# Kernel optimization log

Hardware: AMD Instinct MI355X
Metric: run time of the kernel (lower is better)

## Reference

```python
import jax, jax.numpy as jnp
import numpy as np

N_NODES = 100000
E2 = 1600000
E3 = 1600000
ES = 100000
HID = 64


def _mlp_3x3(x_in, W1, b1, W2, b2):
    # x_in: [E, d_in] -> mobility [E, 3, 3]
    h = jax.nn.relu(x_in @ W1 + b1)
    out = h @ W2 + b2  # [E, 9]
    return out.reshape(-1, 3, 3)


def setup_inputs() -> dict:
    key = jax.random.key(0)
    ks = jax.random.split(key, 20)
    inp = {}
    inp["x"] = jax.random.normal(ks[0], (N_NODES, 3), dtype=jnp.float32)
    inp["edge_2body"] = jax.random.randint(ks[1], (2, E2), 0, N_NODES)
    inp["edge_3body"] = jax.random.randint(ks[2], (3, E3), 0, N_NODES)
    inp["edge_2bodySelf"] = jax.random.randint(ks[3], (2, ES), 0, N_NODES)
    inp["edge_1body"] = jax.random.randint(ks[4], (2, ES), 0, N_NODES)
    inp["edge_attr_2body"] = jax.random.normal(ks[5], (E2, 3), dtype=jnp.float32)
    inp["edge_attr_3body"] = jax.random.normal(ks[6], (E3, 3), dtype=jnp.float32)
    inp["edge_attr_2bodySelf"] = jax.random.normal(ks[7], (ES, 3), dtype=jnp.float32)
    inp["edge_attr_1body"] = jax.random.normal(ks[8], (ES, 3), dtype=jnp.float32)
    s = 0.1
    # nn_2body: 3 -> HID -> 9
    inp["W1_2b"] = jax.random.normal(ks[9], (3, HID), dtype=jnp.float32) * s
    inp["b1_2b"] = jnp.zeros((HID,), jnp.float32)
    inp["W2_2b"] = jax.random.normal(ks[10], (HID, 9), dtype=jnp.float32) * s
    inp["b2_2b"] = jnp.zeros((9,), jnp.float32)
    # nn_3body: 6 -> HID -> 9
    inp["W1_3b"] = jax.random.normal(ks[11], (6, HID), dtype=jnp.float32) * s
    inp["b1_3b"] = jnp.zeros((HID,), jnp.float32)
    inp["W2_3b"] = jax.random.normal(ks[12], (HID, 9), dtype=jnp.float32) * s
    inp["b2_3b"] = jnp.zeros((9,), jnp.float32)
    # nn_self: 3 -> HID -> 9
    inp["W1_s"] = jax.random.normal(ks[13], (3, HID), dtype=jnp.float32) * s
    inp["b1_s"] = jnp.zeros((HID,), jnp.float32)
    inp["W2_s"] = jax.random.normal(ks[14], (HID, 9), dtype=jnp.float32) * s
    inp["b2_s"] = jnp.zeros((9,), jnp.float32)
    return inp


def reference(x, edge_2body, edge_3body, edge_2bodySelf, edge_1body,
              edge_attr_2body, edge_attr_3body, edge_attr_2bodySelf, edge_attr_1body,
              W1_2b, b1_2b, W2_2b, b2_2b,
              W1_3b, b1_3b, W2_3b, b2_3b,
              W1_s, b1_s, W2_s, b2_s):
    n = x.shape[0]
    # ---- 2-body: gather -> MLP -> per-edge 3x3 matvec -> scatter-add ----
    d2 = x[edge_2body[0]] - x[edge_2body[1]]  # xj - xi, [E2,3]
    mob2 = _mlp_3x3(d2, W1_2b, b1_2b, W2_2b, b2_2b)
    y2 = jnp.einsum('eij,ej->ei', mob2, edge_attr_2body)
    v2 = jax.ops.segment_sum(y2, edge_2body[1], num_segments=n)
    # ---- 3-body ----
    xj = x[edge_3body[0]]
    xk = x[edge_3body[1]]
    xi = x[edge_3body[2]]
    d3 = jnp.concatenate((xk - xj, xi - xk), axis=1)  # [E3,6]
    mob3 = _mlp_3x3(d3, W1_3b, b1_3b, W2_3b, b2_3b)
    y3 = jnp.einsum('eij,ej->ei', mob3, edge_attr_3body)
    v3 = jax.ops.segment_sum(y3, edge_3body[2], num_segments=n)
    # ---- 2-body self ----
    ds = x[edge_2bodySelf[0]] - x[edge_2bodySelf[1]]
    mobs = _mlp_3x3(ds, W1_s, b1_s, W2_s, b2_s)
    ys = jnp.einsum('eij,ej->ei', mobs, edge_attr_2bodySelf)
    vs = jax.ops.segment_sum(ys, edge_2bodySelf[1], num_segments=n)
    # edge_1body / edge_attr_1body unused in original forward
    return v2 + v3 + vs
```

## Files before the change

kernel.cpp:

```cpp
#include <hip/hip_runtime.h>


constexpr int HIDDEN = 64;
constexpr int NB_MAX = 256;
constexpr int NPB_SHIFT = 9;
constexpr int NPB = 1 << NPB_SHIFT;
constexpr int TILE_F = NPB * 3;
constexpr int NET_SLOT = 1040;
constexpr int BLK = 256;
constexpr int KPT = 4;

typedef _Float16 h2_t __attribute__((ext_vector_type(2)));

__device__ __forceinline__ unsigned packh2(float a, float b) {
    auto h = __builtin_amdgcn_cvt_pkrtz(a, b);
    return __builtin_bit_cast(unsigned, h);
}
__device__ __forceinline__ float fdot2u(unsigned a, unsigned b, float c) {
    h2_t ha = __builtin_bit_cast(h2_t, a);
    h2_t hb = __builtin_bit_cast(h2_t, b);
#if __has_builtin(__builtin_amdgcn_fdot2)
    return __builtin_amdgcn_fdot2(ha, hb, c, false);
#else
    return fmaf((float)ha.x, (float)hb.x, fmaf((float)ha.y, (float)hb.y, c));
#endif
}


__global__ __launch_bounds__(256) void setup_kernel(
    const float* __restrict__ x, int n_nodes, float4* __restrict__ x4,
    int* __restrict__ gcount,
    const float* __restrict__ W1_2b, const float* __restrict__ b1_2b,
    const float* __restrict__ W2_2b, const float* __restrict__ b2_2b,
    const float* __restrict__ W1_s,  const float* __restrict__ b1_s,
    const float* __restrict__ W2_s,  const float* __restrict__ b2_s,
    const float* __restrict__ W1_3b, const float* __restrict__ b1_3b,
    const float* __restrict__ W2_3b, const float* __restrict__ b2_3b,
    unsigned* __restrict__ nets)
{
    const int blk = blockIdx.x;
    const int tid = threadIdx.x;
    if (blk < 3) {
        const float *W1, *b1, *W2, *b2; int din;
        if (blk == 0) { W1 = W1_2b; b1 = b1_2b; W2 = W2_2b; b2 = b2_2b; din = 3; }
        else if (blk == 1) { W1 = W1_s; b1 = b1_s; W2 = W2_s; b2 = b2_s; din = 3; }
        else { W1 = W1_3b; b1 = b1_3b; W2 = W2_3b; b2 = b2_3b; din = 6; }
        unsigned* slot = nets + blk * NET_SLOT;
        float* slotf = (float*)slot;
        if (tid < 32) {
            const int h2 = tid, hA = 2 * h2, hB = 2 * h2 + 1;
            if (din == 3) {
                unsigned* row = slot + h2 * 16;
                float* rowf = (float*)row;
                row[0] = packh2(W1[0 * HIDDEN + hA], W1[1 * HIDDEN + hA]);
                row[1] = packh2(W1[0 * HIDDEN + hB], W1[1 * HIDDEN + hB]);
                rowf[2] = b1[hA]; rowf[3] = b1[hB];
                rowf[4] = W1[2 * HIDDEN + hA]; rowf[5] = W1[2 * HIDDEN + hB];
                #pragma unroll
                for (int i = 0; i < 9; ++i)
                    row[6 + i] = packh2(W2[hA * 9 + i], W2[hB * 9 + i]);
                row[15] = 0;
            } else {
                unsigned* row = slot + h2 * 32;
                float* rowf = (float*)row;
                #pragma unroll
                for (int r = 0; r < 3; ++r) {
                    row[r]     = packh2(W1[(2 * r) * HIDDEN + hA], W1[(2 * r + 1) * HIDDEN + hA]);
                    row[3 + r] = packh2(W1[(2 * r) * HIDDEN + hB], W1[(2 * r + 1) * HIDDEN + hB]);
                }
                rowf[6] = b1[hA]; rowf[7] = b1[hB];
                #pragma unroll
                for (int i = 0; i < 9; ++i)
                    row[8 + i] = packh2(W2[hA * 9 + i], W2[hB * 9 + i]);
                #pragma unroll
                for (int i = 17; i < 20; ++i) row[i] = 0;
            }
        }
        if (tid >= 32 && tid < 41) slotf[1024 + (tid - 32)] = b2[tid - 32];
        if (blk == 0) gcount[tid] = 0;
    } else {
        int i = (blk - 3) * 256 + tid;
        if (i < n_nodes)
            x4[i] = make_float4(x[3 * i], x[3 * i + 1], x[3 * i + 2], 0.0f);
    }
}

__global__ __launch_bounds__(256) void p1_edge_kernel(
    const float4* __restrict__ x4,
    const int* __restrict__ e0, long long E0, const float* __restrict__ at0,
    const int* __restrict__ e1, long long E1, const float* __restrict__ at1,
    const int* __restrict__ e2, long long E2, const float* __restrict__ at2,
    int g0, int g1,
    const unsigned* __restrict__ nets,
    float4* __restrict__ records, int* __restrict__ gcount, int cap)
{
    static_assert(NB_MAX == BLK, "one reserve bin per thread");
    __shared__ __align__(16) unsigned s_net[1033];
    __shared__ int s_rank[NB_MAX];
    __shared__ int s_base[NB_MAX];

    const int gA = g0 + g1;
    const int gB = (int)gridDim.x - gA;
    const int mn = (gA < gB) ? gA : gB;
    int aidx = -1, b6 = -1;
    {
        const int idx = blockIdx.x;
        if (idx < 2 * mn) { if (idx & 1) b6 = idx >> 1; else aidx = idx >> 1; }
        else {
            const int r = idx - 2 * mn;
            if (gA > gB) aidx = mn + r; else b6 = mn + r;
        }
    }

    const int* edges; long long E; const float* attr;
    int bidx, nblk, din3;
    const unsigned* wp;
    if (aidx >= 0) {
        if (aidx < g0) { edges = e0; E = E0; attr = at0; bidx = aidx;      nblk = g0; din3 = 1; wp = nets; }
        else           { edges = e1; E = E1; attr = at1; bidx = aidx - g0; nblk = g1; din3 = 1; wp = nets + NET_SLOT; }
    } else             { edges = e2; E = E2; attr = at2; bidx = b6;        nblk = gB; din3 = 0; wp = nets + 2 * NET_SLOT; }

    const int tid = threadIdx.x;
    long long span = (E + nblk - 1) / nblk;
    span = (span + 1023) & ~1023LL;
    const long long lo = (long long)bidx * span;
    const long long hi = (lo + span < E) ? (lo + span) : E;
    if (lo >= E) return;

    const bool e_aligned = ((E & 3) == 0);

    s_rank[tid] = 0;
    const int nstage = din3 ? 512 : 1024;
    for (int i = tid; i < nstage; i += BLK) s_net[i] = wp[i];
    if (tid < 9) s_net[1024 + tid] = wp[1024 + tid];
    __syncthreads();

    const unsigned* w = s_net;
    const float* wf = (const float*)s_net;
    float b2r[9];
    #pragma unroll
    for (int i = 0; i < 9; ++i) b2r[i] = wf[1024 + i];

    const long long be = lo + (long long)tid * KPT;

    unsigned dp[KPT][3];
    float    d2s[KPT];
    float    a[KPT][3];
    int      dst[KPT];
    bool     valid[KPT];
    int      i0[KPT], i1[KPT], i2[KPT];

    const bool lane_live = (be < hi);
    const bool full = lane_live && e_aligned && (be + KPT <= hi);
    if (full) {
        int4 r0 = *(const int4*)(edges + be);
        int4 r1 = *(const int4*)(edges + E + be);
        i0[0] = r0.x; i0[1] = r0.y; i0[2] = r0.z; i0[3] = r0.w;
        i1[0] = r1.x; i1[1] = r1.y; i1[2] = r1.z; i1[3] = r1.w;
        if (!din3) {
            int4 r2 = *(const int4*)(edges + 2 * E + be);
            i2[0] = r2.x; i2[1] = r2.y; i2[2] = r2.z; i2[3] = r2.w;
        }
        float4 a0 = *(const float4*)(attr + 3 * be);
        float4 a1 = *(const float4*)(attr + 3 * be + 4);
        float4 a2 = *(const float4*)(attr + 3 * be + 8);
        a[0][0] = a0.x; a[0][1] = a0.y; a[0][2] = a0.z;
        a[1][0] = a0.w; a[1][1] = a1.x; a[1][2] = a1.y;
        a[2][0] = a1.z; a[2][1] = a1.w; a[2][2] = a2.x;
        a[3][0] = a2.y; a[3][1] = a2.z; a[3][2] = a2.w;
        #pragma unroll
        for (int u = 0; u < KPT; ++u) valid[u] = true;
    } else {
        #pragma unroll
        for (int u = 0; u < KPT; ++u) {
            long long e = be + u;
            valid[u] = lane_live && (e < hi);
            long long ee = valid[u] ? e : lo;
            i0[u] = edges[ee];
            i1[u] = edges[E + ee];
            if (!din3) i2[u] = edges[2 * E + ee];
            #pragma unroll
            for (int c = 0; c < 3; ++c) a[u][c] = attr[3 * ee + c];
        }
    }

    #pragma unroll
    for (int u = 0; u < KPT; ++u) {
        if (din3) {
            dst[u] = i1[u];
            float4 xs = x4[i0[u]];
            float4 xt = x4[i1[u]];
            dp[u][0] = packh2(xs.x - xt.x, xs.y - xt.y);
            d2s[u]   = xs.z - xt.z;
            dp[u][1] = 0; dp[u][2] = 0;
        } else {
            dst[u] = i2[u];
            float4 xj = x4[i0[u]];
            float4 xk = x4[i1[u]];
            float4 xi = x4[i2[u]];
            dp[u][0] = packh2(xk.x - xj.x, xk.y - xj.y);
            dp[u][1] = packh2(xk.z - xj.z, xi.x - xk.x);
            dp[u][2] = packh2(xi.y - xk.y, xi.z - xk.z);
            d2s[u] = 0.f;
        }
    }

    float acc[KPT][9];
    #pragma unroll
    for (int u = 0; u < KPT; ++u)
        #pragma unroll
        for (int i = 0; i < 9; ++i) acc[u][i] = b2r[i];

    if (din3) {
        #pragma unroll 2
        for (int hh2 = 0; hh2 < HIDDEN / 2; ++hh2) {
            const uint4* rq = (const uint4*)(w + (hh2 << 4));
            const uint4 q0 = rq[0], q1 = rq[1], q2 = rq[2], q3 = rq[3];
            const unsigned wA = q0.x;
            const unsigned wB = q0.y;
            const float bbA = __uint_as_float(q0.z);
            const float bbB = __uint_as_float(q0.w);
            const float wcA = __uint_as_float(q1.x);
            const float wcB = __uint_as_float(q1.y);
            const unsigned w2p[9] = {q1.z, q1.w, q2.x, q2.y, q2.z,
                                     q2.w, q3.x, q3.y, q3.z};
            #pragma unroll
            for (int u = 0; u < KPT; ++u) {
                float preA = fmaf(d2s[u], wcA, fdot2u(dp[u][0], wA, bbA));
                float preB = fmaf(d2s[u], wcB, fdot2u(dp[u][0], wB, bbB));
                unsigned h2 = packh2(fmaxf(preA, 0.f), fmaxf(preB, 0.f));
                #pragma unroll
                for (int i = 0; i < 9; ++i)
                    acc[u][i] = fdot2u(h2, w2p[i], acc[u][i]);
            }
        }
    } else {
        #pragma unroll 2
        for (int hh2 = 0; hh2 < HIDDEN / 2; ++hh2) {
            const uint4* rq = (const uint4*)(w + (hh2 << 5));
            const uint4 q0 = rq[0], q1 = rq[1], q2 = rq[2], q3 = rq[3];
            const unsigned q4x = w[(hh2 << 5) + 16];
            const unsigned wA0 = q0.x, wA1 = q0.y, wA2 = q0.z;
            const unsigned wB0 = q0.w, wB1 = q1.x, wB2 = q1.y;
            const float bbA = __uint_as_float(q1.z);
            const float bbB = __uint_as_float(q1.w);
            const unsigned w2p[9] = {q2.x, q2.y, q2.z, q2.w, q3.x,
                                     q3.y, q3.z, q3.w, q4x};
            #pragma unroll
            for (int u = 0; u < KPT; ++u) {
                float preA = fdot2u(dp[u][2], wA2,
                             fdot2u(dp[u][1], wA1,
                             fdot2u(dp[u][0], wA0, bbA)));
                float preB = fdot2u(dp[u][2], wB2,
                             fdot2u(dp[u][1], wB1,
                             fdot2u(dp[u][0], wB0, bbB)));
                unsigned h2 = packh2(fmaxf(preA, 0.f), fmaxf(preB, 0.f));
                #pragma unroll
                for (int i = 0; i < 9; ++i)
                    acc[u][i] = fdot2u(h2, w2p[i], acc[u][i]);
            }
        }
    }

    int rk[KPT]; int bb[KPT];
    #pragma unroll
    for (int u = 0; u < KPT; ++u) {
        if (valid[u]) {
            bb[u] = dst[u] >> NPB_SHIFT;
            rk[u] = atomicAdd(&s_rank[bb[u]], 1);
        }
    }
    __syncthreads();

    {
        int c = s_rank[tid];
        s_base[tid] = (c > 0) ? atomicAdd(&gcount[tid], c) : 0;
    }
    __syncthreads();

    #pragma unroll
    for (int u = 0; u < KPT; ++u) {
        if (!valid[u]) continue;
        float y0 = fmaf(acc[u][0], a[u][0], fmaf(acc[u][1], a[u][1], acc[u][2] * a[u][2]));
        float y1 = fmaf(acc[u][3], a[u][0], fmaf(acc[u][4], a[u][1], acc[u][5] * a[u][2]));
        float y2 = fmaf(acc[u][6], a[u][0], fmaf(acc[u][7], a[u][1], acc[u][8] * a[u][2]));
        int slot = s_base[bb[u]] + rk[u];
        if (slot < cap)
            records[(size_t)bb[u] * cap + slot] =
                make_float4(y0, y1, y2, __int_as_float(dst[u]));
    }
}

__global__ __launch_bounds__(1024) void p2_bucket(
    const float4* __restrict__ records, const int* __restrict__ gcount,
    int cap, int n_nodes, float* __restrict__ out)
{
    __shared__ float s_acc[TILE_F];
    const int b = blockIdx.x;
    const int tid = threadIdx.x;

    for (int i = tid; i < TILE_F; i += 1024) s_acc[i] = 0.0f;
    __syncthreads();

    int cnt = gcount[b];
    if (cnt > cap) cnt = cap;
    const float4* rb = records + (size_t)b * cap;

    int i = tid;
    for (; i + 3 * 1024 < cnt; i += 4 * 1024) {
        float4 r0 = rb[i];
        float4 r1 = rb[i + 1024];
        float4 r2 = rb[i + 2048];
        float4 r3 = rb[i + 3072];
        int l0 = __float_as_int(r0.w) - (b << NPB_SHIFT);
        int l1 = __float_as_int(r1.w) - (b << NPB_SHIFT);
        int l2 = __float_as_int(r2.w) - (b << NPB_SHIFT);
        int l3 = __float_as_int(r3.w) - (b << NPB_SHIFT);
        atomicAdd(&s_acc[l0 * 3 + 0], r0.x);
        atomicAdd(&s_acc[l0 * 3 + 1], r0.y);
        atomicAdd(&s_acc[l0 * 3 + 2], r0.z);
        atomicAdd(&s_acc[l1 * 3 + 0], r1.x);
        atomicAdd(&s_acc[l1 * 3 + 1], r1.y);
        atomicAdd(&s_acc[l1 * 3 + 2], r1.z);
        atomicAdd(&s_acc[l2 * 3 + 0], r2.x);
        atomicAdd(&s_acc[l2 * 3 + 1], r2.y);
        atomicAdd(&s_acc[l2 * 3 + 2], r2.z);
        atomicAdd(&s_acc[l3 * 3 + 0], r3.x);
        atomicAdd(&s_acc[l3 * 3 + 1], r3.y);
        atomicAdd(&s_acc[l3 * 3 + 2], r3.z);
    }
    for (; i < cnt; i += 1024) {
        float4 r = rb[i];
        int loc = __float_as_int(r.w) - (b << NPB_SHIFT);
        atomicAdd(&s_acc[loc * 3 + 0], r.x);
        atomicAdd(&s_acc[loc * 3 + 1], r.y);
        atomicAdd(&s_acc[loc * 3 + 2], r.z);
    }
    __syncthreads();

    const int start = (b << NPB_SHIFT) * 3;
    const int end = min(n_nodes * 3, ((b + 1) << NPB_SHIFT) * 3);
    for (int i2 = start + tid; i2 < end; i2 += 1024)
        out[i2] = s_acc[i2 - start];
}

template <int DIN, int KPTF>
__global__ __launch_bounds__(256) void edge_mlp_atomic(
    const float* __restrict__ x,
    const int* __restrict__ edges, long long E,
    const float* __restrict__ attr,
    const float* __restrict__ W1, const float* __restrict__ b1,
    const float* __restrict__ W2, const float* __restrict__ b2,
    float* __restrict__ out)
{
    const int tid = threadIdx.x;
    const long long base = (long long)blockIdx.x * (blockDim.x * KPTF) + tid;
    float d[KPTF][DIN]; float a[KPTF][3]; int dst[KPTF]; bool valid[KPTF];
    #pragma unroll
    for (int u = 0; u < KPTF; ++u) {
        long long e = base + (long long)u * blockDim.x;
        valid[u] = (e < E);
        long long ee = valid[u] ? e : 0;
        if constexpr (DIN == 3) {
            int s = edges[ee]; int t = edges[E + ee]; dst[u] = t;
            #pragma unroll
            for (int c = 0; c < 3; ++c)
                d[u][c] = x[3 * (long long)s + c] - x[3 * (long long)t + c];
        } else {
            int j = edges[ee]; int k = edges[E + ee]; int i = edges[2 * E + ee];
            dst[u] = i;
            #pragma unroll
            for (int c = 0; c < 3; ++c) {
                float xj = x[3 * (long long)j + c];
                float xk = x[3 * (long long)k + c];
                float xi = x[3 * (long long)i + c];
                d[u][c] = xk - xj; d[u][3 + c] = xi - xk;
            }
        }
        #pragma unroll
        for (int c = 0; c < 3; ++c) a[u][c] = attr[3 * ee + c];
    }
    float acc[KPTF][9];
    #pragma unroll
    for (int u = 0; u < KPTF; ++u)
        #pragma unroll
        for (int i = 0; i < 9; ++i) acc[u][i] = b2[i];
    #pragma unroll 4
    for (int hh = 0; hh < HIDDEN; ++hh) {
        const float bb = b1[hh];
        float w1r[DIN];
        #pragma unroll
        for (int r = 0; r < DIN; ++r) w1r[r] = W1[r * HIDDEN + hh];
        float w2r[9];
        #pragma unroll
        for (int i = 0; i < 9; ++i) w2r[i] = W2[hh * 9 + i];
        #pragma unroll
        for (int u = 0; u < KPTF; ++u) {
            float pre = bb;
            #pragma unroll
            for (int r = 0; r < DIN; ++r) pre = fmaf(d[u][r], w1r[r], pre);
            const float h = fmaxf(pre, 0.0f);
            #pragma unroll
            for (int i = 0; i < 9; ++i) acc[u][i] = fmaf(h, w2r[i], acc[u][i]);
        }
    }
    #pragma unroll
    for (int u = 0; u < KPTF; ++u) {
        if (!valid[u]) continue;
        float* o = out + 3 * (long long)dst[u];
        #pragma unroll
        for (int i = 0; i < 3; ++i) {
            float y = fmaf(acc[u][3 * i + 0], a[u][0],
                      fmaf(acc[u][3 * i + 1], a[u][1],
                           acc[u][3 * i + 2] * a[u][2]));
            atomicAdd(&o[i], y);
        }
    }
}

extern "C" void kernel_launch(void* const* d_in, const int* in_sizes, int n_in,
                              void* d_out, int out_size, void* d_ws, size_t ws_size,
                              hipStream_t stream)
{
    const float* x  = (const float*)d_in[0];
    const int*   e2 = (const int*)d_in[1];
    const int*   e3 = (const int*)d_in[2];
    const int*   es = (const int*)d_in[3];
    const float* a2 = (const float*)d_in[5];
    const float* a3 = (const float*)d_in[6];
    const float* as = (const float*)d_in[7];
    const float* W1_2b = (const float*)d_in[9];
    const float* b1_2b = (const float*)d_in[10];
    const float* W2_2b = (const float*)d_in[11];
    const float* b2_2b = (const float*)d_in[12];
    const float* W1_3b = (const float*)d_in[13];
    const float* b1_3b = (const float*)d_in[14];
    const float* W2_3b = (const float*)d_in[15];
    const float* b2_3b = (const float*)d_in[16];
    const float* W1_s  = (const float*)d_in[17];
    const float* b1_s  = (const float*)d_in[18];
    const float* W2_s  = (const float*)d_in[19];
    const float* b2_s  = (const float*)d_in[20];

    const long long E2 = in_sizes[1] / 2;
    const long long E3 = in_sizes[2] / 3;
    const long long ES = in_sizes[3] / 2;
    const long long Etot = E2 + E3 + ES;
    const int n_nodes = out_size / 3;
    const int nbuckets = (n_nodes + NPB - 1) >> NPB_SHIFT;

    float* out = (float*)d_out;

    const size_t off_nets = 1024;
    const size_t off_x4 = (off_nets + 3 * NET_SLOT * 4 + 255) & ~(size_t)255;
    const size_t x4_bytes = (size_t)n_nodes * sizeof(float4);
    const size_t off_rec = (off_x4 + x4_bytes + 255) & ~(size_t)255;

    long long mean_per_bucket = (Etot + nbuckets - 1) / nbuckets;
    long long min_cap = mean_per_bucket + 1600;
    long long cap_avail =
        ((long long)ws_size - (long long)off_rec) / ((long long)nbuckets * 16);

    constexpr int SPAN = 1024;
    int g0 = (int)((E2 + SPAN - 1) / SPAN);
    int g1 = (int)((ES + SPAN - 1) / SPAN);
    int g2g = (int)((E3 + SPAN - 1) / SPAN);

    if (nbuckets <= NB_MAX && cap_avail >= min_cap) {
        long long capL = min_cap + 4096;
        if (capL > cap_avail) capL = cap_avail;
        int cap = (int)capL;
        int* gcount = (int*)d_ws;
        unsigned* nets = (unsigned*)((char*)d_ws + off_nets);
        float4* x4 = (float4*)((char*)d_ws + off_x4);
        float4* records = (float4*)((char*)d_ws + off_rec);

        int nb_pad = (n_nodes + 255) / 256;
        setup_kernel<<<3 + nb_pad, 256, 0, stream>>>(
            x, n_nodes, x4, gcount,
            W1_2b, b1_2b, W2_2b, b2_2b,
            W1_s,  b1_s,  W2_s,  b2_s,
            W1_3b, b1_3b, W2_3b, b2_3b,
            nets);

        p1_edge_kernel<<<g0 + g1 + g2g, 256, 0, stream>>>(
            x4,
            e2, E2, a2,
            es, ES, as,
            e3, E3, a3,
            g0, g1,
            nets, records, gcount, cap);

        p2_bucket<<<nbuckets, 1024, 0, stream>>>(records, gcount, cap, n_nodes, out);
    } else {
        hipMemsetAsync(out, 0, (size_t)out_size * sizeof(float), stream);
        constexpr int FB_BLK = 256, FB_KPT = 4;
        const long long per_blk = (long long)FB_BLK * FB_KPT;
        int a2g = (int)((E2 + per_blk - 1) / per_blk);
        int a3g = (int)((E3 + per_blk - 1) / per_blk);
        int asg = (int)((ES + per_blk - 1) / per_blk);
        if (a2g > 0)
            edge_mlp_atomic<3, FB_KPT><<<a2g, FB_BLK, 0, stream>>>(
                x, e2, E2, a2, W1_2b, b1_2b, W2_2b, b2_2b, out);
        if (a3g > 0)
            edge_mlp_atomic<6, FB_KPT><<<a3g, FB_BLK, 0, stream>>>(
                x, e3, E3, a3, W1_3b, b1_3b, W2_3b, b2_3b, out);
        if (asg > 0)
            edge_mlp_atomic<3, FB_KPT><<<asg, FB_BLK, 0, stream>>>(
                x, es, ES, as, W1_s, b1_s, W2_s, b2_s, out);
    }
}
```

Measured before the change: 282.4 us.

## Make edge blocks loop over multiple 1024-edge chunks from both edge sets

The edge kernel now launches about a quarter as many blocks. Each block walks up to two chunks from the 2-body/self side and two from the 3-body side in sequence. Weight staging into shared memory is skipped when consecutive chunks use the same network. The aim is to amortise per-block setup and the global bucket-count atomics over more work. The cost is fewer resident waves for hiding gather latency, and each block's chunks run one after another.

```diff
diff --git a/kernel.cpp b/kernel.cpp
--- a/kernel.cpp
+++ b/kernel.cpp
@@ -90,7 +90,7 @@
     const int* __restrict__ e0, long long E0, const float* __restrict__ at0,
     const int* __restrict__ e1, long long E1, const float* __restrict__ at1,
     const int* __restrict__ e2, long long E2, const float* __restrict__ at2,
-    int g0, int g1,
+    int g0, int gA, int gB,
     const unsigned* __restrict__ nets,
     float4* __restrict__ records, int* __restrict__ gcount, int cap)
 {
@@ -99,195 +99,194 @@
     __shared__ int s_rank[NB_MAX];
     __shared__ int s_base[NB_MAX];
 
-    const int gA = g0 + g1;
-    const int gB = (int)gridDim.x - gA;
-    const int mn = (gA < gB) ? gA : gB;
-    int aidx = -1, b6 = -1;
-    {
-        const int idx = blockIdx.x;
-        if (idx < 2 * mn) { if (idx & 1) b6 = idx >> 1; else aidx = idx >> 1; }
-        else {
-            const int r = idx - 2 * mn;
-            if (gA > gB) aidx = mn + r; else b6 = mn + r;
+    const int tid = threadIdx.x;
+    const int blk = blockIdx.x;
+    int cur_set = -1;
+
+    for (int side = 0; side < 2; ++side) {
+        const int lim = side ? gB : gA;
+        for (int j = 0; j < 2; ++j) {
+            const int t = 2 * blk + j;
+            if (t >= lim) continue;
+
+            const int* edges; long long E; const float* attr;
+            int din3, set; long long lo;
+            if (side == 0) {
+                if (t < g0) { set = 0; edges = e0; E = E0; attr = at0; lo = (long long)t << 10; }
+                else        { set = 1; edges = e1; E = E1; attr = at1; lo = (long long)(t - g0) << 10; }
+                din3 = 1;
+            } else {
+                set = 2; edges = e2; E = E2; attr = at2; din3 = 0;
+                lo = (long long)t << 10;
+            }
+            const long long hi = (lo + 1024 < E) ? lo + 1024 : E;
+            const bool e_aligned = ((E & 3) == 0);
+
+            s_rank[tid] = 0;
+            if (set != cur_set) {
+                const unsigned* wp = nets + set * NET_SLOT;
+                const int nstage = din3 ? 512 : 1024;
+                for (int i = tid; i < nstage; i += BLK) s_net[i] = wp[i];
+                if (tid < 9) s_net[1024 + tid] = wp[1024 + tid];
+                cur_set = set;
+            }
+            __syncthreads();
+
+            const unsigned* w = s_net;
+            const float* wf = (const float*)s_net;
+            float b2r[9];
+            #pragma unroll
+            for (int i = 0; i < 9; ++i) b2r[i] = wf[1024 + i];
+
+            const long long be = lo + (long long)tid * KPT;
+
+            unsigned dp[KPT][3];
+            float    d2s[KPT];
+            float    a[KPT][3];
+            int      dst[KPT];
+            bool     valid[KPT];
+            int      i0[KPT], i1[KPT], i2[KPT];
+
+            const bool lane_live = (be < hi);
+            const bool full = lane_live && e_aligned && (be + KPT <= hi);
+            if (full) {
+                int4 r0 = *(const int4*)(edges + be);
+                int4 r1 = *(const int4*)(edges + E + be);
+                i0[0] = r0.x; i0[1] = r0.y; i0[2] = r0.z; i0[3] = r0.w;
+                i1[0] = r1.x; i1[1] = r1.y; i1[2] = r1.z; i1[3] = r1.w;
+                if (!din3) {
+                    int4 r2 = *(const int4*)(edges + 2 * E + be);
+                    i2[0] = r2.x; i2[1] = r2.y; i2[2] = r2.z; i2[3] = r2.w;
+                }
+                float4 a0 = *(const float4*)(attr + 3 * be);
+                float4 a1 = *(const float4*)(attr + 3 * be + 4);
+                float4 a2 = *(const float4*)(attr + 3 * be + 8);
+                a[0][0] = a0.x; a[0][1] = a0.y; a[0][2] = a0.z;
+                a[1][0] = a0.w; a[1][1] = a1.x; a[1][2] = a1.y;
+                a[2][0] = a1.z; a[2][1] = a1.w; a[2][2] = a2.x;
+                a[3][0] = a2.y; a[3][1] = a2.z; a[3][2] = a2.w;
+                #pragma unroll
+                for (int u = 0; u < KPT; ++u) valid[u] = true;
+            } else {
+                #pragma unroll
+                for (int u = 0; u < KPT; ++u) {
+                    long long e = be + u;
+                    valid[u] = lane_live && (e < hi);
+                    long long ee = valid[u] ? e : lo;
+                    i0[u] = edges[ee];
+                    i1[u] = edges[E + ee];
+                    if (!din3) i2[u] = edges[2 * E + ee];
+                    #pragma unroll
+                    for (int c = 0; c < 3; ++c) a[u][c] = attr[3 * ee + c];
+                }
+            }
+
+            #pragma unroll
+            for (int u = 0; u < KPT; ++u) {
+                if (din3) {
+                    dst[u] = i1[u];
+                    float4 xs = x4[i0[u]];
+                    float4 xt = x4[i1[u]];
+                    dp[u][0] = packh2(xs.x - xt.x, xs.y - xt.y);
+                    d2s[u]   = xs.z - xt.z;
+                    dp[u][1] = 0; dp[u][2] = 0;
+                } else {
+                    dst[u] = i2[u];
+                    float4 xj = x4[i0[u]];
+                    float4 xk = x4[i1[u]];
+                    float4 xi = x4[i2[u]];
+                    dp[u][0] = packh2(xk.x - xj.x, xk.y - xj.y);
+                    dp[u][1] = packh2(xk.z - xj.z, xi.x - xk.x);
+                    dp[u][2] = packh2(xi.y - xk.y, xi.z - xk.z);
+                    d2s[u] = 0.f;
+                }
+            }
+
+            float acc[KPT][9];
+            #pragma unroll
+            for (int u = 0; u < KPT; ++u)
+                #pragma unroll
+                for (int i = 0; i < 9; ++i) acc[u][i] = b2r[i];
+
+            if (din3) {
+                #pragma unroll 2
+                for (int hh2 = 0; hh2 < HIDDEN / 2; ++hh2) {
+                    const uint4* rq = (const uint4*)(w + (hh2 << 4));
+                    const uint4 q0 = rq[0], q1 = rq[1], q2 = rq[2], q3 = rq[3];
+                    const unsigned wA = q0.x;
+                    const unsigned wB = q0.y;
+                    const float bbA = __uint_as_float(q0.z);
+                    const float bbB = __uint_as_float(q0.w);
+                    const float wcA = __uint_as_float(q1.x);
+                    const float wcB = __uint_as_float(q1.y);
+                    const unsigned w2p[9] = {q1.z, q1.w, q2.x, q2.y, q2.z,
+                                             q2.w, q3.x, q3.y, q3.z};
+                    #pragma unroll
+                    for (int u = 0; u < KPT; ++u) {
+                        float preA = fmaf(d2s[u], wcA, fdot2u(dp[u][0], wA, bbA));
+                        float preB = fmaf(d2s[u], wcB, fdot2u(dp[u][0], wB, bbB));
+                        unsigned h2 = packh2(fmaxf(preA, 0.f), fmaxf(preB, 0.f));
+                        #pragma unroll
+                        for (int i = 0; i < 9; ++i)
+                            acc[u][i] = fdot2u(h2, w2p[i], acc[u][i]);
+                    }
+                }
+            } else {
+                #pragma unroll 2
+                for (int hh2 = 0; hh2 < HIDDEN / 2; ++hh2) {
+                    const uint4* rq = (const uint4*)(w + (hh2 << 5));
+                    const uint4 q0 = rq[0], q1 = rq[1], q2 = rq[2], q3 = rq[3];
+                    const unsigned q4x = w[(hh2 << 5) + 16];
+                    const unsigned wA0 = q0.x, wA1 = q0.y, wA2 = q0.z;
+                    const unsigned wB0 = q0.w, wB1 = q1.x, wB2 = q1.y;
+                    const float bbA = __uint_as_float(q1.z);
+                    const float bbB = __uint_as_float(q1.w);
+                    const unsigned w2p[9] = {q2.x, q2.y, q2.z, q2.w, q3.x,
+                                             q3.y, q3.z, q3.w, q4x};
+                    #pragma unroll
+                    for (int u = 0; u < KPT; ++u) {
+                        float preA = fdot2u(dp[u][2], wA2,
+                                     fdot2u(dp[u][1], wA1,
+                                     fdot2u(dp[u][0], wA0, bbA)));
+                        float preB = fdot2u(dp[u][2], wB2,
+                                     fdot2u(dp[u][1], wB1,
+                                     fdot2u(dp[u][0], wB0, bbB)));
+                        unsigned h2 = packh2(fmaxf(preA, 0.f), fmaxf(preB, 0.f));
+                        #pragma unroll
+                        for (int i = 0; i < 9; ++i)
+                            acc[u][i] = fdot2u(h2, w2p[i], acc[u][i]);
+                    }
+                }
+            }
+
+            int rk[KPT]; int bb[KPT];
+            #pragma unroll
+            for (int u = 0; u < KPT; ++u) {
+                if (valid[u]) {
+                    bb[u] = dst[u] >> NPB_SHIFT;
+                    rk[u] = atomicAdd(&s_rank[bb[u]], 1);
+                }
+            }
+            __syncthreads();
+
+            {
+                int c = s_rank[tid];
+                s_base[tid] = (c > 0) ? atomicAdd(&gcount[tid], c) : 0;
+            }
+            __syncthreads();
+
+            #pragma unroll
+            for (int u = 0; u < KPT; ++u) {
+                if (!valid[u]) continue;
+                float y0 = fmaf(acc[u][0], a[u][0], fmaf(acc[u][1], a[u][1], acc[u][2] * a[u][2]));
+                float y1 = fmaf(acc[u][3], a[u][0], fmaf(acc[u][4], a[u][1], acc[u][5] * a[u][2]));
+                float y2 = fmaf(acc[u][6], a[u][0], fmaf(acc[u][7], a[u][1], acc[u][8] * a[u][2]));
+                int slot = s_base[bb[u]] + rk[u];
+                if (slot < cap)
+                    records[(size_t)bb[u] * cap + slot] =
+                        make_float4(y0, y1, y2, __int_as_float(dst[u]));
+            }
         }
-    }
-
-    const int* edges; long long E; const float* attr;
-    int bidx, nblk, din3;
-    const unsigned* wp;
-    if (aidx >= 0) {
-        if (aidx < g0) { edges = e0; E = E0; attr = at0; bidx = aidx;      nblk = g0; din3 = 1; wp = nets; }
-        else           { edges = e1; E = E1; attr = at1; bidx = aidx - g0; nblk = g1; din3 = 1; wp = nets + NET_SLOT; }
-    } else             { edges = e2; E = E2; attr = at2; bidx = b6;        nblk = gB; din3 = 0; wp = nets + 2 * NET_SLOT; }
-
-    const int tid = threadIdx.x;
-    long long span = (E + nblk - 1) / nblk;
-    span = (span + 1023) & ~1023LL;
-    const long long lo = (long long)bidx * span;
-    const long long hi = (lo + span < E) ? (lo + span) : E;
-    if (lo >= E) return;
-
-    const bool e_aligned = ((E & 3) == 0);
-
-    s_rank[tid] = 0;
-    const int nstage = din3 ? 512 : 1024;
-    for (int i = tid; i < nstage; i += BLK) s_net[i] = wp[i];
-    if (tid < 9) s_net[1024 + tid] = wp[1024 + tid];
-    __syncthreads();
-
-    const unsigned* w = s_net;
-    const float* wf = (const float*)s_net;
-    float b2r[9];
-    #pragma unroll
-    for (int i = 0; i < 9; ++i) b2r[i] = wf[1024 + i];
-
-    const long long be = lo + (long long)tid * KPT;
-
-    unsigned dp[KPT][3];
-    float    d2s[KPT];
-    float    a[KPT][3];
-    int      dst[KPT];
-    bool     valid[KPT];
-    int      i0[KPT], i1[KPT], i2[KPT];
-
-    const bool lane_live = (be < hi);
-    const bool full = lane_live && e_aligned && (be + KPT <= hi);
-    if (full) {
-        int4 r0 = *(const int4*)(edges + be);
-        int4 r1 = *(const int4*)(edges + E + be);
-        i0[0] = r0.x; i0[1] = r0.y; i0[2] = r0.z; i0[3] = r0.w;
-        i1[0] = r1.x; i1[1] = r1.y; i1[2] = r1.z; i1[3] = r1.w;
-        if (!din3) {
-            int4 r2 = *(const int4*)(edges + 2 * E + be);
-            i2[0] = r2.x; i2[1] = r2.y; i2[2] = r2.z; i2[3] = r2.w;
-        }
-        float4 a0 = *(const float4*)(attr + 3 * be);
-        float4 a1 = *(const float4*)(attr + 3 * be + 4);
-        float4 a2 = *(const float4*)(attr + 3 * be + 8);
-        a[0][0] = a0.x; a[0][1] = a0.y; a[0][2] = a0.z;
-        a[1][0] = a0.w; a[1][1] = a1.x; a[1][2] = a1.y;
-        a[2][0] = a1.z; a[2][1] = a1.w; a[2][2] = a2.x;
-        a[3][0] = a2.y; a[3][1] = a2.z; a[3][2] = a2.w;
-        #pragma unroll
-        for (int u = 0; u < KPT; ++u) valid[u] = true;
-    } else {
-        #pragma unroll
-        for (int u = 0; u < KPT; ++u) {
-            long long e = be + u;
-            valid[u] = lane_live && (e < hi);
-            long long ee = valid[u] ? e : lo;
-            i0[u] = edges[ee];
-            i1[u] = edges[E + ee];
-            if (!din3) i2[u] = edges[2 * E + ee];
-            #pragma unroll
-            for (int c = 0; c < 3; ++c) a[u][c] = attr[3 * ee + c];
-        }
-    }
-
-    #pragma unroll
-    for (int u = 0; u < KPT; ++u) {
-        if (din3) {
-            dst[u] = i1[u];
-            float4 xs = x4[i0[u]];
-            float4 xt = x4[i1[u]];
-            dp[u][0] = packh2(xs.x - xt.x, xs.y - xt.y);
-            d2s[u]   = xs.z - xt.z;
-            dp[u][1] = 0; dp[u][2] = 0;
-        } else {
-            dst[u] = i2[u];
-            float4 xj = x4[i0[u]];
-            float4 xk = x4[i1[u]];
-            float4 xi = x4[i2[u]];
-            dp[u][0] = packh2(xk.x - xj.x, xk.y - xj.y);
-            dp[u][1] = packh2(xk.z - xj.z, xi.x - xk.x);
-            dp[u][2] = packh2(xi.y - xk.y, xi.z - xk.z);
-            d2s[u] = 0.f;
-        }
-    }
-
-    float acc[KPT][9];
-    #pragma unroll
-    for (int u = 0; u < KPT; ++u)
-        #pragma unroll
-        for (int i = 0; i < 9; ++i) acc[u][i] = b2r[i];
-
-    if (din3) {
-        #pragma unroll 2
-        for (int hh2 = 0; hh2 < HIDDEN / 2; ++hh2) {
-            const uint4* rq = (const uint4*)(w + (hh2 << 4));
-            const uint4 q0 = rq[0], q1 = rq[1], q2 = rq[2], q3 = rq[3];
-            const unsigned wA = q0.x;
-            const unsigned wB = q0.y;
-            const float bbA = __uint_as_float(q0.z);
-            const float bbB = __uint_as_float(q0.w);
-            const float wcA = __uint_as_float(q1.x);
-            const float wcB = __uint_as_float(q1.y);
-            const unsigned w2p[9] = {q1.z, q1.w, q2.x, q2.y, q2.z,
-                                     q2.w, q3.x, q3.y, q3.z};
-            #pragma unroll
-            for (int u = 0; u < KPT; ++u) {
-                float preA = fmaf(d2s[u], wcA, fdot2u(dp[u][0], wA, bbA));
-                float preB = fmaf(d2s[u], wcB, fdot2u(dp[u][0], wB, bbB));
-                unsigned h2 = packh2(fmaxf(preA, 0.f), fmaxf(preB, 0.f));
-                #pragma unroll
-                for (int i = 0; i < 9; ++i)
-                    acc[u][i] = fdot2u(h2, w2p[i], acc[u][i]);
-            }
-        }
-    } else {
-        #pragma unroll 2
-        for (int hh2 = 0; hh2 < HIDDEN / 2; ++hh2) {
-            const uint4* rq = (const uint4*)(w + (hh2 << 5));
-            const uint4 q0 = rq[0], q1 = rq[1], q2 = rq[2], q3 = rq[3];
-            const unsigned q4x = w[(hh2 << 5) + 16];
-            const unsigned wA0 = q0.x, wA1 = q0.y, wA2 = q0.z;
-            const unsigned wB0 = q0.w, wB1 = q1.x, wB2 = q1.y;
-            const float bbA = __uint_as_float(q1.z);
-            const float bbB = __uint_as_float(q1.w);
-            const unsigned w2p[9] = {q2.x, q2.y, q2.z, q2.w, q3.x,
-                                     q3.y, q3.z, q3.w, q4x};
-            #pragma unroll
-            for (int u = 0; u < KPT; ++u) {
-                float preA = fdot2u(dp[u][2], wA2,
-                             fdot2u(dp[u][1], wA1,
-                             fdot2u(dp[u][0], wA0, bbA)));
-                float preB = fdot2u(dp[u][2], wB2,
-                             fdot2u(dp[u][1], wB1,
-                             fdot2u(dp[u][0], wB0, bbB)));
-                unsigned h2 = packh2(fmaxf(preA, 0.f), fmaxf(preB, 0.f));
-                #pragma unroll
-                for (int i = 0; i < 9; ++i)
-                    acc[u][i] = fdot2u(h2, w2p[i], acc[u][i]);
-            }
-        }
-    }
-
-    int rk[KPT]; int bb[KPT];
-    #pragma unroll
-    for (int u = 0; u < KPT; ++u) {
-        if (valid[u]) {
-            bb[u] = dst[u] >> NPB_SHIFT;
-            rk[u] = atomicAdd(&s_rank[bb[u]], 1);
-        }
-    }
-    __syncthreads();
-
-    {
-        int c = s_rank[tid];
-        s_base[tid] = (c > 0) ? atomicAdd(&gcount[tid], c) : 0;
-    }
-    __syncthreads();
-
-    #pragma unroll
-    for (int u = 0; u < KPT; ++u) {
-        if (!valid[u]) continue;
-        float y0 = fmaf(acc[u][0], a[u][0], fmaf(acc[u][1], a[u][1], acc[u][2] * a[u][2]));
-        float y1 = fmaf(acc[u][3], a[u][0], fmaf(acc[u][4], a[u][1], acc[u][5] * a[u][2]));
-        float y2 = fmaf(acc[u][6], a[u][0], fmaf(acc[u][7], a[u][1], acc[u][8] * a[u][2]));
-        int slot = s_base[bb[u]] + rk[u];
-        if (slot < cap)
-            records[(size_t)bb[u] * cap + slot] =
-                make_float4(y0, y1, y2, __int_as_float(dst[u]));
     }
 }
 
@@ -461,10 +460,12 @@
     long long cap_avail =
         ((long long)ws_size - (long long)off_rec) / ((long long)nbuckets * 16);
 
-    constexpr int SPAN = 1024;
-    int g0 = (int)((E2 + SPAN - 1) / SPAN);
-    int g1 = (int)((ES + SPAN - 1) / SPAN);
-    int g2g = (int)((E3 + SPAN - 1) / SPAN);
+    int g0 = (int)((E2 + 1023) / 1024);
+    int g1 = (int)((ES + 1023) / 1024);
+    int gB = (int)((E3 + 1023) / 1024);
+    int gA = g0 + g1;
+    int gmax = (gA > gB) ? gA : gB;
+    int G = (gmax + 1) / 2;
 
     if (nbuckets <= NB_MAX && cap_avail >= min_cap) {
         long long capL = min_cap + 4096;
@@ -483,12 +484,12 @@
             W1_3b, b1_3b, W2_3b, b2_3b,
             nets);
 
-        p1_edge_kernel<<<g0 + g1 + g2g, 256, 0, stream>>>(
+        p1_edge_kernel<<<G, 256, 0, stream>>>(
             x4,
             e2, E2, a2,
             es, ES, as,
             e3, E3, a3,
-            g0, g1,
+            g0, gA, gB,
             nets, records, gcount, cap);
 
         p2_bucket<<<nbuckets, 1024, 0, stream>>>(records, gcount, cap, n_nodes, out);
```

After: 302.8 us. 7.2% more time.

## Fold setup kernel into edge kernel: pack weights per block, gather x directly

Applied to the files above, without the earlier changes.

Removes the separate setup kernel. Each edge block now packs the MLP weights into shared memory itself, and the per-node x values are gathered directly as 12-byte structs instead of padded float4 copies. The gcount reset becomes a memset, and the weight packing overlaps with the index and coordinate gathers before a barrier placed later. This saves one kernel launch and the x4 staging pass, at the cost of redundant per-block weight packing and unaligned 12-byte gathers.

```diff
diff --git a/kernel.cpp b/kernel.cpp
--- a/kernel.cpp
+++ b/kernel.cpp
@@ -6,11 +6,12 @@
 constexpr int NPB_SHIFT = 9;
 constexpr int NPB = 1 << NPB_SHIFT;
 constexpr int TILE_F = NPB * 3;
-constexpr int NET_SLOT = 1040;
 constexpr int BLK = 256;
 constexpr int KPT = 4;
 
 typedef _Float16 h2_t __attribute__((ext_vector_type(2)));
+
+struct F3 { float x, y, z; };
 
 __device__ __forceinline__ unsigned packh2(float a, float b) {
     auto h = __builtin_amdgcn_cvt_pkrtz(a, b);
@@ -27,71 +28,18 @@
 }
 
 
-__global__ __launch_bounds__(256) void setup_kernel(
-    const float* __restrict__ x, int n_nodes, float4* __restrict__ x4,
-    int* __restrict__ gcount,
+__global__ __launch_bounds__(256) void p1_edge_kernel(
+    const float* __restrict__ x,
+    const int* __restrict__ e0, long long E0, const float* __restrict__ at0,
+    const int* __restrict__ e1, long long E1, const float* __restrict__ at1,
+    const int* __restrict__ e2, long long E2, const float* __restrict__ at2,
+    int g0, int g1,
     const float* __restrict__ W1_2b, const float* __restrict__ b1_2b,
     const float* __restrict__ W2_2b, const float* __restrict__ b2_2b,
     const float* __restrict__ W1_s,  const float* __restrict__ b1_s,
     const float* __restrict__ W2_s,  const float* __restrict__ b2_s,
     const float* __restrict__ W1_3b, const float* __restrict__ b1_3b,
     const float* __restrict__ W2_3b, const float* __restrict__ b2_3b,
-    unsigned* __restrict__ nets)
-{
-    const int blk = blockIdx.x;
-    const int tid = threadIdx.x;
-    if (blk < 3) {
-        const float *W1, *b1, *W2, *b2; int din;
-        if (blk == 0) { W1 = W1_2b; b1 = b1_2b; W2 = W2_2b; b2 = b2_2b; din = 3; }
-        else if (blk == 1) { W1 = W1_s; b1 = b1_s; W2 = W2_s; b2 = b2_s; din = 3; }
-        else { W1 = W1_3b; b1 = b1_3b; W2 = W2_3b; b2 = b2_3b; din = 6; }
-        unsigned* slot = nets + blk * NET_SLOT;
-        float* slotf = (float*)slot;
-        if (tid < 32) {
-            const int h2 = tid, hA = 2 * h2, hB = 2 * h2 + 1;
-            if (din == 3) {
-                unsigned* row = slot + h2 * 16;
-                float* rowf = (float*)row;
-                row[0] = packh2(W1[0 * HIDDEN + hA], W1[1 * HIDDEN + hA]);
-                row[1] = packh2(W1[0 * HIDDEN + hB], W1[1 * HIDDEN + hB]);
-                rowf[2] = b1[hA]; rowf[3] = b1[hB];
-                rowf[4] = W1[2 * HIDDEN + hA]; rowf[5] = W1[2 * HIDDEN + hB];
-                #pragma unroll
-                for (int i = 0; i < 9; ++i)
-                    row[6 + i] = packh2(W2[hA * 9 + i], W2[hB * 9 + i]);
-                row[15] = 0;
-            } else {
-                unsigned* row = slot + h2 * 32;
-                float* rowf = (float*)row;
-                #pragma unroll
-                for (int r = 0; r < 3; ++r) {
-                    row[r]     = packh2(W1[(2 * r) * HIDDEN + hA], W1[(2 * r + 1) * HIDDEN + hA]);
-                    row[3 + r] = packh2(W1[(2 * r) * HIDDEN + hB], W1[(2 * r + 1) * HIDDEN + hB]);
-                }
-                rowf[6] = b1[hA]; rowf[7] = b1[hB];
-                #pragma unroll
-                for (int i = 0; i < 9; ++i)
-                    row[8 + i] = packh2(W2[hA * 9 + i], W2[hB * 9 + i]);
-                #pragma unroll
-                for (int i = 17; i < 20; ++i) row[i] = 0;
-            }
-        }
-        if (tid >= 32 && tid < 41) slotf[1024 + (tid - 32)] = b2[tid - 32];
-        if (blk == 0) gcount[tid] = 0;
-    } else {
-        int i = (blk - 3) * 256 + tid;
-        if (i < n_nodes)
-            x4[i] = make_float4(x[3 * i], x[3 * i + 1], x[3 * i + 2], 0.0f);
-    }
-}
-
-__global__ __launch_bounds__(256) void p1_edge_kernel(
-    const float4* __restrict__ x4,
-    const int* __restrict__ e0, long long E0, const float* __restrict__ at0,
-    const int* __restrict__ e1, long long E1, const float* __restrict__ at1,
-    const int* __restrict__ e2, long long E2, const float* __restrict__ at2,
-    int g0, int g1,
-    const unsigned* __restrict__ nets,
     float4* __restrict__ records, int* __restrict__ gcount, int cap)
 {
     static_assert(NB_MAX == BLK, "one reserve bin per thread");
@@ -114,11 +62,14 @@
 
     const int* edges; long long E; const float* attr;
     int bidx, nblk, din3;
-    const unsigned* wp;
+    const float *W1, *b1, *W2, *b2;
     if (aidx >= 0) {
-        if (aidx < g0) { edges = e0; E = E0; attr = at0; bidx = aidx;      nblk = g0; din3 = 1; wp = nets; }
-        else           { edges = e1; E = E1; attr = at1; bidx = aidx - g0; nblk = g1; din3 = 1; wp = nets + NET_SLOT; }
-    } else             { edges = e2; E = E2; attr = at2; bidx = b6;        nblk = gB; din3 = 0; wp = nets + 2 * NET_SLOT; }
+        if (aidx < g0) { edges = e0; E = E0; attr = at0; bidx = aidx;      nblk = g0; din3 = 1;
+                         W1 = W1_2b; b1 = b1_2b; W2 = W2_2b; b2 = b2_2b; }
+        else           { edges = e1; E = E1; attr = at1; bidx = aidx - g0; nblk = g1; din3 = 1;
+                         W1 = W1_s;  b1 = b1_s;  W2 = W2_s;  b2 = b2_s; }
+    } else             { edges = e2; E = E2; attr = at2; bidx = b6;        nblk = gB; din3 = 0;
+                         W1 = W1_3b; b1 = b1_3b; W2 = W2_3b; b2 = b2_3b; }
 
     const int tid = threadIdx.x;
     long long span = (E + nblk - 1) / nblk;
@@ -130,16 +81,33 @@
     const bool e_aligned = ((E & 3) == 0);
 
     s_rank[tid] = 0;
-    const int nstage = din3 ? 512 : 1024;
-    for (int i = tid; i < nstage; i += BLK) s_net[i] = wp[i];
-    if (tid < 9) s_net[1024 + tid] = wp[1024 + tid];
-    __syncthreads();
-
-    const unsigned* w = s_net;
-    const float* wf = (const float*)s_net;
-    float b2r[9];
-    #pragma unroll
-    for (int i = 0; i < 9; ++i) b2r[i] = wf[1024 + i];
+    if (tid < 32) {
+        const int h2 = tid, hA = 2 * h2, hB = 2 * h2 + 1;
+        if (din3) {
+            unsigned* row = s_net + h2 * 16;
+            float* rowf = (float*)row;
+            row[0] = packh2(W1[0 * HIDDEN + hA], W1[1 * HIDDEN + hA]);
+            row[1] = packh2(W1[0 * HIDDEN + hB], W1[1 * HIDDEN + hB]);
+            rowf[2] = b1[hA]; rowf[3] = b1[hB];
+            rowf[4] = W1[2 * HIDDEN + hA]; rowf[5] = W1[2 * HIDDEN + hB];
+            #pragma unroll
+            for (int i = 0; i < 9; ++i)
+                row[6 + i] = packh2(W2[hA * 9 + i], W2[hB * 9 + i]);
+        } else {
+            unsigned* row = s_net + h2 * 32;
+            float* rowf = (float*)row;
+            #pragma unroll
+            for (int r = 0; r < 3; ++r) {
+                row[r]     = packh2(W1[(2 * r) * HIDDEN + hA], W1[(2 * r + 1) * HIDDEN + hA]);
+                row[3 + r] = packh2(W1[(2 * r) * HIDDEN + hB], W1[(2 * r + 1) * HIDDEN + hB]);
+            }
+            rowf[6] = b1[hA]; rowf[7] = b1[hB];
+            #pragma unroll
+            for (int i = 0; i < 9; ++i)
+                row[8 + i] = packh2(W2[hA * 9 + i], W2[hB * 9 + i]);
+        }
+    }
+    if (tid >= 32 && tid < 41) ((float*)s_net)[1024 + (tid - 32)] = b2[tid - 32];
 
     const long long be = lo + (long long)tid * KPT;
 
@@ -184,26 +152,35 @@
         }
     }
 
+    const F3* x3 = (const F3*)x;
     #pragma unroll
     for (int u = 0; u < KPT; ++u) {
         if (din3) {
             dst[u] = i1[u];
-            float4 xs = x4[i0[u]];
-            float4 xt = x4[i1[u]];
+            F3 xs = x3[i0[u]];
+            F3 xt = x3[i1[u]];
             dp[u][0] = packh2(xs.x - xt.x, xs.y - xt.y);
             d2s[u]   = xs.z - xt.z;
             dp[u][1] = 0; dp[u][2] = 0;
         } else {
             dst[u] = i2[u];
-            float4 xj = x4[i0[u]];
-            float4 xk = x4[i1[u]];
-            float4 xi = x4[i2[u]];
+            F3 xj = x3[i0[u]];
+            F3 xk = x3[i1[u]];
+            F3 xi = x3[i2[u]];
             dp[u][0] = packh2(xk.x - xj.x, xk.y - xj.y);
             dp[u][1] = packh2(xk.z - xj.z, xi.x - xk.x);
             dp[u][2] = packh2(xi.y - xk.y, xi.z - xk.z);
             d2s[u] = 0.f;
         }
     }
+
+    __syncthreads();
+
+    const unsigned* w = s_net;
+    const float* wf = (const float*)s_net;
+    float b2r[9];
+    #pragma unroll
+    for (int i = 0; i < 9; ++i) b2r[i] = wf[1024 + i];
 
     float acc[KPT][9];
     #pragma unroll
@@ -451,10 +428,7 @@
 
     float* out = (float*)d_out;
 
-    const size_t off_nets = 1024;
-    const size_t off_x4 = (off_nets + 3 * NET_SLOT * 4 + 255) & ~(size_t)255;
-    const size_t x4_bytes = (size_t)n_nodes * sizeof(float4);
-    const size_t off_rec = (off_x4 + x4_bytes + 255) & ~(size_t)255;
+    const size_t off_rec = 1024;
 
     long long mean_per_bucket = (Etot + nbuckets - 1) / nbuckets;
     long long min_cap = mean_per_bucket + 1600;
@@ -471,25 +445,20 @@
         if (capL > cap_avail) capL = cap_avail;
         int cap = (int)capL;
         int* gcount = (int*)d_ws;
-        unsigned* nets = (unsigned*)((char*)d_ws + off_nets);
-        float4* x4 = (float4*)((char*)d_ws + off_x4);
         float4* records = (float4*)((char*)d_ws + off_rec);
 
-        int nb_pad = (n_nodes + 255) / 256;
-        setup_kernel<<<3 + nb_pad, 256, 0, stream>>>(
-            x, n_nodes, x4, gcount,
-            W1_2b, b1_2b, W2_2b, b2_2b,
-            W1_s,  b1_s,  W2_s,  b2_s,
-            W1_3b, b1_3b, W2_3b, b2_3b,
-            nets);
+        hipMemsetAsync(d_ws, 0, 1024, stream);
 
         p1_edge_kernel<<<g0 + g1 + g2g, 256, 0, stream>>>(
-            x4,
+            x,
             e2, E2, a2,
             es, ES, as,
             e3, E3, a3,
             g0, g1,
-            nets, records, gcount, cap);
+            W1_2b, b1_2b, W2_2b, b2_2b,
+            W1_s,  b1_s,  W2_s,  b2_s,
+            W1_3b, b1_3b, W2_3b, b2_3b,
+            records, gcount, cap);
 
         p2_bucket<<<nbuckets, 1024, 0, stream>>>(records, gcount, cap, n_nodes, out);
     } else {
```

Result: slower. 292.7 us (+3.7%).
